# Optimization experiments

Measured on AMD Instinct MI355X. Metric: run time of the kernel, lower is better.

The kernel has to match this reference:

```python
import jax, jax.numpy as jnp
import numpy as np
from jax import lax

RF = 19       # receptive field: layers*(kernel-1)+1 = 3*6+1
WINDOW = 12
N_MIX = 2
K = 20        # subgraph_size (top-k per row)
GDEP = 2
ALPHA = 0.05  # propalpha
EPS = 1e-5


def conv2d(x, w, b):
    # x: [N,C,H,W], w: [O,I,1,k], valid conv along time (last) axis
    o = lax.conv_general_dilated(x, w, (1, 1), 'VALID',
                                 dimension_numbers=('NCHW', 'OIHW', 'NCHW'))
    return o + b[None, :, None, None]


def dilated_inception(x, ws, b):
    # ws: kernels [co, ci, k] for k in (2,3,6,7); dilation factor is 1 here
    outs = [lax.conv_general_dilated(x, w[:, :, None, :], (1, 1), 'VALID',
                                     dimension_numbers=('NCHW', 'OIHW', 'NCHW'))
            for w in ws]
    L = outs[-1].shape[-1]  # truncate to shortest (largest kernel) length
    out = jnp.concatenate([o[..., -L:] for o in outs], axis=1)
    return out + b[None, :, None, None]


def build_adj(e1, e2, l1w, l1b, l2w, l2b):
    # e1,e2: [M2,N,D] embedding tables (idx = arange -> full table)
    # torch Linear: y = x @ W.T + b, W: [out,in]
    nv1 = jnp.einsum('mnd,mod->mno', e1, l1w) + l1b[:, None, :]
    nv2 = jnp.einsum('mnd,mod->mno', e2, l2w) + l2b[:, None, :]
    a = jnp.einsum('mnd,mkd->mnk', nv1, nv2)  # [M2, N, N] per-block adjacency
    rows = [jnp.concatenate([a[i * N_MIX + j] for j in range(N_MIX)], axis=1)
            for i in range(N_MIX)]
    adj = jnp.concatenate(rows, axis=0)  # [NT, NT]
    _, t = lax.top_k(adj, K)  # per-row top-k indices
    mask = jnp.zeros_like(adj).at[jnp.arange(adj.shape[0])[:, None], t].set(1.0)
    return adj * mask


def mixprop(x, adj, w, b):
    a = adj + jnp.eye(adj.shape[0], dtype=adj.dtype)
    a = a / jnp.sum(a, axis=1, keepdims=True)  # row-normalize
    h = x
    outs = [h]
    for _ in range(GDEP):
        h = ALPHA * x + (1.0 - ALPHA) * jnp.einsum('ncwl,vw->ncvl', h, a)
        outs.append(h)
    ho = jnp.concatenate(outs, axis=1)  # [B,(GDEP+1)*C,V,L]
    return jnp.einsum('ncvl,oc->novl', ho, w) + b[None, :, None, None]


def layernorm(x, w, b):
    # torch F.layer_norm over all dims except batch; idx = arange -> full affine
    mu = jnp.mean(x, axis=(1, 2, 3), keepdims=True)
    var = jnp.mean((x - mu) ** 2, axis=(1, 2, 3), keepdims=True)
    return (x - mu) * lax.rsqrt(var + EPS) * w[None] + b[None]


def setup_inputs() -> dict:
    keys = iter(jax.random.split(jax.random.key(0), 80))
    def rn(shape, s=0.1):
        return s * jax.random.normal(next(keys), shape, dtype=jnp.float32)
    d = {}
    d['x_in'] = jax.random.normal(next(keys), (32, 12, 500, 4), dtype=jnp.float32)
    d['start_w'] = rn((32, 1, 1, 1)); d['start_b'] = rn((32,))
    d['skip0_w'] = rn((64, 1, 1, 19)); d['skip0_b'] = rn((64,))
    d['emb1'] = rn((3, 4, 500, 40)); d['emb2'] = rn((3, 4, 500, 40))
    d['lin1_w'] = rn((3, 4, 40, 40)); d['lin1_b'] = rn((3, 4, 40))
    d['lin2_w'] = rn((3, 4, 40, 40)); d['lin2_b'] = rn((3, 4, 40))
    d['g1_w'] = rn((3, 32, 96)); d['g1_b'] = rn((3, 32))
    d['g2_w'] = rn((3, 32, 96)); d['g2_b'] = rn((3, 32))
    for pref in ('filt', 'gate'):
        for k in (2, 3, 6, 7):
            d[f'{pref}_w{k}'] = rn((3, 8, 32, k))
        d[f'{pref}_b'] = rn((3, 32))
    for i, L in zip((1, 2, 3), (13, 7, 1)):
        d[f'skip_w{i}'] = rn((64, 32, 1, L)); d[f'skip_b{i}'] = rn((64,))
        d[f'norm_w{i}'] = jnp.ones((32, 1000, L), jnp.float32)
        d[f'norm_b{i}'] = jnp.zeros((32, 1000, L), jnp.float32)
    d['skipE_w'] = rn((64, 32, 1, 1)); d['skipE_b'] = rn((64,))
    d['end1_w'] = rn((128, 64, 1, 1)); d['end1_b'] = rn((128,))
    d['end2_w'] = rn((12, 128, 1, 1)); d['end2_b'] = rn((12,))
    return d


def reference(x_in, start_w, start_b, skip0_w, skip0_b, emb1, emb2,
              lin1_w, lin1_b, lin2_w, lin2_b, g1_w, g1_b, g2_w, g2_b,
              filt_w2, filt_w3, filt_w6, filt_w7, filt_b,
              gate_w2, gate_w3, gate_w6, gate_w7, gate_b,
              skip_w1, skip_b1, skip_w2, skip_b2, skip_w3, skip_b3,
              norm_w1, norm_b1, norm_w2, norm_b2, norm_w3, norm_b3,
              skipE_w, skipE_b, end1_w, end1_b, end2_w, end2_b):
    feat = x_in[..., :-2]  # drop last 2 'time' features
    # split per-mode feature and stack along node dim: [B,T,2N,1]
    inp = jnp.concatenate([feat[..., 0:1], feat[..., 1:2]], axis=2)
    inp = jnp.transpose(inp, (0, 3, 2, 1))  # [B,1,2N,T]
    inp = jnp.pad(inp, ((0, 0), (0, 0), (0, 0), (RF - WINDOW, 0)))
    x = conv2d(inp, start_w, start_b)       # [B,32,1000,19]
    skip = conv2d(inp, skip0_w, skip0_b)    # [B,64,1000,1] (dropout=eval no-op)
    filt_ws = (filt_w2, filt_w3, filt_w6, filt_w7)
    gate_ws = (gate_w2, gate_w3, gate_w6, gate_w7)
    skips = ((skip_w1, skip_b1), (skip_w2, skip_b2), (skip_w3, skip_b3))
    norms = ((norm_w1, norm_b1), (norm_w2, norm_b2), (norm_w3, norm_b3))
    for i in range(3):
        adp = build_adj(emb1[i], emb2[i], lin1_w[i], lin1_b[i], lin2_w[i], lin2_b[i])
        residual = x
        x = mixprop(x, adp, g1_w[i], g1_b[i]) + mixprop(x, adp.T, g2_w[i], g2_b[i])
        f = jnp.tanh(dilated_inception(x, [w[i] for w in filt_ws], filt_b[i]))
        g = jax.nn.sigmoid(dilated_inception(x, [w[i] for w in gate_ws], gate_b[i]))
        x = f * g
        sw, sb = skips[i]
        skip = conv2d(x, sw, sb) + skip
        x = x + residual[..., -x.shape[3]:]
        nw, nb = norms[i]
        x = layernorm(x, nw, nb)
    skip = conv2d(x, skipE_w, skipE_b) + skip
    x = jax.nn.relu(skip)
    x = jax.nn.relu(conv2d(x, end1_w, end1_b))
    return conv2d(x, end2_w, end2_b)  # [B, horizon*out_dim0=12, 1000, 1]
```

## Files before the change

kernel.cpp:

```cpp
#include <hip/hip_runtime.h>
#include <math.h>


#define ALPHA_C 0.05f
#define EPS_C 1e-5f
#define NBC 32
#define CSCT_CAP 140000

__device__ float g_inp[32 * 19 * 1000];
__device__ float g_skip[32 * 64 * 1000];
__device__ float g_nv1[240000];
__device__ float g_nv2[240000];
__device__ __align__(16) int   g_tkcol[60000];
__device__ __align__(16) float g_tkval[60000];
__device__ float g_inv1[3000];
__device__ int   g_colcnt[3000];
__device__ float g_colsum[3000];
__device__ int   g_rp2[3 * 1001 + 1];
__device__ int   g_fill[3000];
__device__ int   g_cscr[60000];
__device__ float g_cscv[60000];
__device__ float g_inv2[3000];
__device__ float g_stats[3 * 64];
__device__ __align__(16) int2 g_pk1T[60000];
__device__ __align__(16) int2 g_cscT[3 * CSCT_CAP];
__device__ int   g_perm[3 * 1024];
__device__ int   g_degT[3 * 1024];
__device__ int   g_iperm[3 * 1000];
__device__ int   g_tOff[3 * 17];
__device__ float g_B0[(size_t)NBC * 32 * 19 * 1000];
__device__ float g_B1[(size_t)NBC * 32 * 19 * 1000];
__device__ float g_B2[(size_t)NBC * 32 * 19 * 1000];
__device__ float g_B3[(size_t)NBC * 32 * 19 * 1000];
__device__ float g_B4[(size_t)NBC * 32 * 19 * 1000];
__device__ float g_B5[(size_t)NBC * 32 * 19 * 1000];

__device__ __forceinline__ float* bufsel(int s)
{
    switch (s) {
        case 0: return g_B0;
        case 1: return g_B1;
        case 2: return g_B2;
        case 3: return g_B3;
        case 4: return g_B4;
        default: return g_B5;
    }
}

__global__ void k_init()
{
    int i = blockIdx.x * 256 + threadIdx.x;
    if (i < 3000) { g_colcnt[i] = 0; g_colsum[i] = 0.f; g_fill[i] = 0; }
    if (i < 192) g_stats[i] = 0.f;
}

__global__ void k_out_zero(float* __restrict__ out, int n)
{
    int i = blockIdx.x * 256 + threadIdx.x;
    if (i < n) out[i] = 0.0f;
}

__global__ void k_marker(float* __restrict__ out, float v)
{
    if (threadIdx.x == 0) out[0] = v;
}


__global__ void k_build_inp(const float* __restrict__ xin)
{
    int i = blockIdx.x * 256 + threadIdx.x;
    if (i >= 32 * 19 * 1000) return;
    int v = i % 1000;
    int t = (i / 1000) % 19;
    int b = i / 19000;
    float val = 0.f;
    if (t >= 7) {
        int tt = t - 7;
        int n = (v < 500) ? v : v - 500;
        int f = (v < 500) ? 0 : 1;
        val = xin[((b * 12 + tt) * 500 + n) * 4 + f];
    }
    g_inp[i] = val;
}

__global__ void k_nv(const float* __restrict__ e1, const float* __restrict__ e2,
                     const float* __restrict__ w1, const float* __restrict__ b1,
                     const float* __restrict__ w2, const float* __restrict__ b2)
{
    int i = blockIdx.x * 256 + threadIdx.x;
    if (i >= 12 * 500 * 40) return;
    int o = i % 40;
    int n = (i / 40) % 500;
    int m = i / (40 * 500);
    const float* p1 = e1 + (m * 500 + n) * 40;
    const float* pw1 = w1 + (m * 40 + o) * 40;
    const float* p2 = e2 + (m * 500 + n) * 40;
    const float* pw2 = w2 + (m * 40 + o) * 40;
    float a1 = b1[m * 40 + o], a2 = b2[m * 40 + o];
    for (int d = 0; d < 40; ++d) {
        a1 += p1[d] * pw1[d];
        a2 += p2[d] * pw2[d];
    }
    g_nv1[i] = a1;
    g_nv2[i] = a2;
}

__global__ __launch_bounds__(256) void k_adj_topk()
{
    __shared__ float row[1000];
    __shared__ float rv[256];
    __shared__ int ri[256];
    __shared__ int selc[20];
    __shared__ float selv[20];
    int li = blockIdx.x / 1000;
    int r = blockIdx.x % 1000;
    int tid = threadIdx.x;
    int bi = r / 500, n = r % 500;
    for (int c = tid; c < 1000; c += 256) {
        int bj = c / 500, k = c % 500;
        int mg = li * 4 + 2 * bi + bj;
        const float* a = g_nv1 + (mg * 500 + n) * 40;
        const float* b = g_nv2 + (mg * 500 + k) * 40;
        float acc = 0.f;
#pragma unroll
        for (int d = 0; d < 40; ++d) acc += a[d] * b[d];
        row[c] = acc;
    }
    __syncthreads();
    for (int sel = 0; sel < 20; ++sel) {
        float bv = -INFINITY;
        int bidx = 0;
        for (int c = tid; c < 1000; c += 256) {
            float x = row[c];
            if (x > bv) { bv = x; bidx = c; }
        }
        rv[tid] = bv;
        ri[tid] = bidx;
        __syncthreads();
        for (int s = 128; s > 0; s >>= 1) {
            if (tid < s) {
                float ov = rv[tid + s];
                int oi = ri[tid + s];
                if (ov > rv[tid] || (ov == rv[tid] && oi < ri[tid])) { rv[tid] = ov; ri[tid] = oi; }
            }
            __syncthreads();
        }
        if (tid == 0) {
            int ci = ri[0];
            if (ci < 0 || ci > 999) ci = sel;
            selc[sel] = ci;
            selv[sel] = rv[0];
            g_tkcol[(li * 1000 + r) * 20 + sel] = ci;
            g_tkval[(li * 1000 + r) * 20 + sel] = rv[0];
            row[ci] = -INFINITY;
        }
        __syncthreads();
    }
    if (tid < 20) {
        atomicAdd(&g_colcnt[li * 1000 + selc[tid]], 1);
        atomicAdd(&g_colsum[li * 1000 + selc[tid]], selv[tid]);
    }
    if (tid == 0) {
        float s = 0.f;
        for (int j = 0; j < 20; ++j) s += selv[j];
        g_inv1[li * 1000 + r] = 1.f / (s + 1.f);
    }
}

__global__ __launch_bounds__(256) void k_scan()
{
    __shared__ int s[1000];
    int li = blockIdx.x;
    int tid = threadIdx.x;
    for (int i = tid; i < 1000; i += 256) s[i] = g_colcnt[li * 1000 + i];
    __syncthreads();
    if (tid == 0) {
        int run = 0;
        for (int i = 0; i < 1000; ++i) { int c = s[i]; s[i] = run; run += c; }
        g_rp2[li * 1001 + 1000] = run;
    }
    __syncthreads();
    for (int i = tid; i < 1000; i += 256) {
        g_rp2[li * 1001 + i] = s[i];
        g_inv2[li * 1000 + i] = 1.f / (g_colsum[li * 1000 + i] + 1.f);
    }
}

__global__ __launch_bounds__(256) void k_permsort()
{
    __shared__ int deg[1000];
    __shared__ int tmax[16];
    int li = blockIdx.x;
    int tid = threadIdx.x;
    for (int v = tid; v < 1000; v += 256)
        deg[v] = g_rp2[li * 1001 + v + 1] - g_rp2[li * 1001 + v];
    __syncthreads();
    for (int v = tid; v < 1000; v += 256) {
        int d = deg[v];
        int r = 0;
        for (int u = 0; u < 1000; ++u) {
            int du = deg[u];
            r += (du > d) || (du == d && u < v);
        }
        g_perm[li * 1024 + r] = v;
        g_degT[li * 1024 + r] = d;
        g_iperm[li * 1000 + v] = r;
        if ((r & 63) == 0) tmax[r >> 6] = d;
    }
    if (tid < 24) {
        g_perm[li * 1024 + 1000 + tid] = -1;
        g_degT[li * 1024 + 1000 + tid] = 0;
    }
    __syncthreads();
    if (tid == 0) {
        int off = 0;
        for (int t = 0; t < 16; ++t) {
            g_tOff[li * 17 + t] = off;
            off += 64 * tmax[t];
        }
        g_tOff[li * 17 + 16] = off;
    }
}

__global__ void k_scatter()
{
    int i = blockIdx.x * 256 + threadIdx.x;
    if (i >= 3 * 20000) return;
    int li = i / 20000;
    int e = i % 20000;
    int r = e / 20;
    int c = g_tkcol[i];
    if (c < 0) c = 0;
    if (c > 999) c = 999;
    float v = g_tkval[i];
    int pos = g_rp2[li * 1001 + c] + atomicAdd(&g_fill[li * 1000 + c], 1);
    if (pos < 0) pos = 0;
    if (pos > 19999) pos = 19999;
    g_cscr[li * 20000 + pos] = r;
    g_cscv[li * 20000 + pos] = v;
}

__global__ void k_packT1()
{
    int i = blockIdx.x * 256 + threadIdx.x;
    if (i >= 60000) return;
    int li = i / 20000;
    int e = i % 20000;
    int v = e / 20, j = e % 20;
    int c1 = g_tkcol[i];
    if (c1 < 0) c1 = 0;
    if (c1 > 999) c1 = 999;
    g_pk1T[li * 20000 + j * 1000 + v] = make_int2(c1 * 16, __float_as_int(g_tkval[i]));
}

__global__ void k_packT2()
{
    int i = blockIdx.x * 256 + threadIdx.x;
    if (i >= 3000) return;
    int li = i / 1000, v = i % 1000;
    int r = g_iperm[li * 1000 + v];
    int t = r >> 6, ln = r & 63;
    int j0 = g_rp2[li * 1001 + v];
    int d = g_rp2[li * 1001 + v + 1] - j0;
    int base = g_tOff[li * 17 + t];
    for (int j = 0; j < d; ++j) {
        int row = g_cscr[li * 20000 + j0 + j];
        if (row < 0) row = 0;
        if (row > 999) row = 999;
        int pos = base + j * 64 + ln;
        if (pos >= 0 && pos < CSCT_CAP)
            g_cscT[li * CSCT_CAP + pos] =
                make_int2(row * 16, __float_as_int(g_cscv[li * 20000 + j0 + j]));
    }
}


__global__ void k_start(const float* __restrict__ sw, const float* __restrict__ sb, int xsel)
{
    float* X = bufsel(xsel);
    long long i = (long long)blockIdx.x * 256 + threadIdx.x;
    if (i >= (long long)NBC * 32 * 19 * 1000) return;
    int v = (int)(i % 1000);
    int t = (int)((i / 1000) % 19);
    int c = (int)((i / 19000) % 32);
    int bl = (int)(i / (19000LL * 32));
    X[i] = sw[c] * g_inp[(bl * 19 + t) * 1000 + v] + sb[c];
}

__global__ __launch_bounds__(256) void k_skip0(const float* __restrict__ w,
                                               const float* __restrict__ bb)
{
    __shared__ float s_inp[19 * 32];
    __shared__ float s_w[64 * 19];
    int b = blockIdx.y;
    int v0 = blockIdx.x * 32;
    int tid = threadIdx.x;
    for (int i = tid; i < 64 * 19; i += 256) s_w[i] = w[i];
    for (int i = tid; i < 19 * 32; i += 256) {
        int t = i / 32, vl = i % 32;
        int v = v0 + vl;
        s_inp[i] = (v < 1000) ? g_inp[(b * 19 + t) * 1000 + v] : 0.f;
    }
    __syncthreads();
    for (int e = tid; e < 64 * 32; e += 256) {
        int o = e / 32, vl = e % 32;
        int v = v0 + vl;
        if (v >= 1000) continue;
        float acc = bb[o];
#pragma unroll
        for (int t = 0; t < 19; ++t) acc += s_w[o * 19 + t] * s_inp[t * 32 + vl];
        g_skip[(b * 64 + o) * 1000 + v] = acc;
    }
}

__global__ __launch_bounds__(256, 5) void k_prop4(int xsel, int o1s, int o2s, int o3s, int o4s,
                                                  int li, int CH)
{
    __shared__ float4 S[2000];
    const float* X = bufsel(xsel);
    float* o1 = bufsel(o1s);
    float* o2 = bufsel(o2s);
    float* o3 = bufsel(o3s);
    float* o4 = bufsel(o4s);
    const int2* pkT = g_pk1T + li * 20000;
    const int2* cT = g_cscT + (size_t)li * CSCT_CAP;
    const int* prm = g_perm + li * 1024;
    const int* dgT = g_degT + li * 1024;
    const int* tOf = g_tOff + li * 17;
    const float* iv1 = g_inv1 + li * 1000;
    const float* iv2 = g_inv2 + li * 1000;
    int n = blockIdx.y;
    int ch0 = blockIdx.x * 4;
    size_t gb = ((size_t)n * CH + ch0) * 1000;
    int tid = threadIdx.x;
    int wv = tid >> 6, lane = tid & 63;
    char* Ub = (char*)S;
    char* Wb = (char*)(S + 1000);
    float4* U4 = S;
    float4* W4 = S + 1000;

    auto csr_hop = [&](const char* sb, float4* dst) {
        for (int it = 0; it < 4; ++it) {
            int v = it * 256 + tid;
            if (v >= 1000) break;
            const int2* mp = pkT + v;
            float4 a = *(const float4*)(sb + (size_t)v * 16);
#pragma unroll
            for (int jb = 0; jb < 5; ++jb) {
                int2 e0 = mp[(jb * 4 + 0) * 1000];
                int2 e1 = mp[(jb * 4 + 1) * 1000];
                int2 e2 = mp[(jb * 4 + 2) * 1000];
                int2 e3 = mp[(jb * 4 + 3) * 1000];
                float w0 = __int_as_float(e0.y), w1 = __int_as_float(e1.y);
                float w2 = __int_as_float(e2.y), w3 = __int_as_float(e3.y);
                float4 x0 = *(const float4*)(sb + e0.x);
                float4 x1 = *(const float4*)(sb + e1.x);
                float4 x2 = *(const float4*)(sb + e2.x);
                float4 x3 = *(const float4*)(sb + e3.x);
                a.x += w0 * x0.x + w1 * x1.x + w2 * x2.x + w3 * x3.x;
                a.y += w0 * x0.y + w1 * x1.y + w2 * x2.y + w3 * x3.y;
                a.z += w0 * x0.z + w1 * x1.z + w2 * x2.z + w3 * x3.z;
                a.w += w0 * x0.w + w1 * x1.w + w2 * x2.w + w3 * x3.w;
            }
            float s = iv1[v];
            a.x *= s; a.y *= s; a.z *= s; a.w *= s;
            dst[v] = a;
        }
    };

    auto csc_hop = [&](const char* sb, float4* dst) {
        for (int o = 0; o < 4; ++o) {
            int tile = o * 4 + ((o & 1) ? (3 - wv) : wv);
            int r = tile * 64 + lane;
            int v = prm[r];
            if (v < 0) continue;
            int d = dgT[r];
            const int2* mp = cT + tOf[tile] + lane;
            float4 a = *(const float4*)(sb + (size_t)v * 16);
            int j = 0;
            for (; j + 4 <= d; j += 4) {
                int2 e0 = mp[(j + 0) * 64];
                int2 e1 = mp[(j + 1) * 64];
                int2 e2 = mp[(j + 2) * 64];
                int2 e3 = mp[(j + 3) * 64];
                float w0 = __int_as_float(e0.y), w1 = __int_as_float(e1.y);
                float w2 = __int_as_float(e2.y), w3 = __int_as_float(e3.y);
                float4 x0 = *(const float4*)(sb + e0.x);
                float4 x1 = *(const float4*)(sb + e1.x);
                float4 x2 = *(const float4*)(sb + e2.x);
                float4 x3 = *(const float4*)(sb + e3.x);
                a.x += w0 * x0.x + w1 * x1.x + w2 * x2.x + w3 * x3.x;
                a.y += w0 * x0.y + w1 * x1.y + w2 * x2.y + w3 * x3.y;
                a.z += w0 * x0.z + w1 * x1.z + w2 * x2.z + w3 * x3.z;
                a.w += w0 * x0.w + w1 * x1.w + w2 * x2.w + w3 * x3.w;
            }
            for (; j < d; ++j) {
                int2 e = mp[j * 64];
                float w = __int_as_float(e.y);
                float4 x = *(const float4*)(sb + e.x);
                a.x += w * x.x; a.y += w * x.y; a.z += w * x.z; a.w += w * x.w;
            }
            float s = iv2[v];
            a.x *= s; a.y *= s; a.z *= s; a.w *= s;
            dst[v] = a;
        }
    };

    for (int it = 0; it < 4; ++it) {
        int v = it * 256 + tid;
        if (v >= 1000) break;
        float4 t;
        t.x = X[gb + v];
        t.y = X[gb + 1000 + v];
        t.z = X[gb + 2000 + v];
        t.w = X[gb + 3000 + v];
        U4[v] = t;
    }
    __syncthreads();

    csr_hop(Ub, W4);
    __syncthreads();

    for (int it = 0; it < 4; ++it) {
        int v = it * 256 + tid;
        if (v >= 1000) break;
        float4 t = W4[v];
        o1[gb + v] = t.x;
        o1[gb + 1000 + v] = t.y;
        o1[gb + 2000 + v] = t.z;
        o1[gb + 3000 + v] = t.w;
    }
    csr_hop(Wb, U4);
    __syncthreads();

    for (int it = 0; it < 4; ++it) {
        int v = it * 256 + tid;
        if (v >= 1000) break;
        float4 t = U4[v];
        o2[gb + v] = t.x;
        o2[gb + 1000 + v] = t.y;
        o2[gb + 2000 + v] = t.z;
        o2[gb + 3000 + v] = t.w;
        float4 x;
        x.x = X[gb + v];
        x.y = X[gb + 1000 + v];
        x.z = X[gb + 2000 + v];
        x.w = X[gb + 3000 + v];
        W4[v] = x;
    }
    __syncthreads();

    csc_hop(Wb, U4);
    __syncthreads();

    for (int it = 0; it < 4; ++it) {
        int v = it * 256 + tid;
        if (v >= 1000) break;
        float4 t = U4[v];
        o3[gb + v] = t.x;
        o3[gb + 1000 + v] = t.y;
        o3[gb + 2000 + v] = t.z;
        o3[gb + 3000 + v] = t.w;
    }
    csc_hop(Ub, W4);
    __syncthreads();

    for (int it = 0; it < 4; ++it) {
        int v = it * 256 + tid;
        if (v >= 1000) break;
        float4 t = W4[v];
        o4[gb + v] = t.x;
        o4[gb + 1000 + v] = t.y;
        o4[gb + 2000 + v] = t.z;
        o4[gb + 3000 + v] = t.w;
    }
}

__global__ __launch_bounds__(256) void k_mix(int xs, int h1s, int h2s, int h3s, int h4s, int ms,
                                             const float* __restrict__ g1w, const float* __restrict__ g2w,
                                             const float* __restrict__ g1b, const float* __restrict__ g2b,
                                             int P)
{
    __shared__ float sW[5 * 1024];
    __shared__ float sB[32];
    int tid = threadIdx.x;
    const float A = ALPHA_C, Bq = 1.f - ALPHA_C;
    for (int i = tid; i < 1024; i += 256) {
        int o = i >> 5, c = i & 31;
        float w1 = g1w[o * 96 + 32 + c], w2 = g1w[o * 96 + 64 + c];
        float w3 = g2w[o * 96 + 32 + c], w4 = g2w[o * 96 + 64 + c];
        sW[i]        = g1w[o * 96 + c] + g2w[o * 96 + c] + A * (w1 + w2 + w3 + w4);
        sW[1024 + i] = Bq * (w1 + A * w2);
        sW[2048 + i] = Bq * Bq * w2;
        sW[3072 + i] = Bq * (w3 + A * w4);
        sW[4096 + i] = Bq * Bq * w4;
    }
    if (tid < 32) sB[tid] = g1b[tid] + g2b[tid];
    __syncthreads();
    int n = blockIdx.y;
    int p = blockIdx.x * 256 + tid;
    if (p >= P) return;
    const float* srcs[5] = {bufsel(xs), bufsel(h1s), bufsel(h2s), bufsel(h3s), bufsel(h4s)};
    float acc[32];
#pragma unroll
    for (int o = 0; o < 32; ++o) acc[o] = sB[o];
    for (int st = 0; st < 5; ++st) {
        const float* src = srcs[st] + (size_t)n * 32 * P + p;
        const float* w = &sW[st * 1024];
        for (int c = 0; c < 32; ++c) {
            float hv = src[(size_t)c * P];
#pragma unroll
            for (int o = 0; o < 32; ++o) acc[o] += w[o * 32 + c] * hv;
        }
    }
    float* XM = bufsel(ms) + (size_t)n * 32 * P + p;
#pragma unroll
    for (int o = 0; o < 32; ++o) XM[(size_t)o * P] = acc[o];
}

template <int LIN>
__global__ __launch_bounds__(256) void k_incept(int xmsel, int xgsel,
                                                const float* __restrict__ fw2, const float* __restrict__ fw3,
                                                const float* __restrict__ fw6, const float* __restrict__ fw7,
                                                const float* __restrict__ fb,
                                                const float* __restrict__ gw2, const float* __restrict__ gw3,
                                                const float* __restrict__ gw6, const float* __restrict__ gw7,
                                                const float* __restrict__ gb,
                                                const float* __restrict__ skw, const float* __restrict__ skb)
{
    const int LOUT = LIN - 6;
    const float* XM = bufsel(xmsel);
    float* XG = bufsel(xgsel);
    __shared__ float sx[32 * 8 * LIN];
    __shared__ float sxg[32 * 8 * LOUT];
    int tid = threadIdx.x;
    int n = blockIdx.y, v0 = blockIdx.x * 8;
    for (int i = tid; i < 32 * LIN * 8; i += 256) {
        int vl = i & 7;
        int l = (i >> 3) % LIN;
        int c = i / (8 * LIN);
        sx[(c * 8 + vl) * LIN + l] = XM[(((size_t)n * 32 + c) * LIN + l) * 1000 + v0 + vl];
    }
    __syncthreads();
    int co = tid >> 3, vl = tid & 7;
    int s = co >> 3, co_s = co & 7;
    const int ksz[4] = {2, 3, 6, 7};
    int k = ksz[s];
    const float* fw = (s == 0) ? fw2 : ((s == 1) ? fw3 : ((s == 2) ? fw6 : fw7));
    const float* gw = (s == 0) ? gw2 : ((s == 1) ? gw3 : ((s == 2) ? gw6 : gw7));
    float accf[LOUT], accg[LOUT];
    float bf = fb[co], bg = gb[co];
#pragma unroll
    for (int l = 0; l < LOUT; ++l) { accf[l] = bf; accg[l] = bg; }
    for (int c = 0; c < 32; ++c) {
        const float* xp = &sx[(c * 8 + vl) * LIN];
        for (int j = 0; j < k; ++j) {
            float wf = fw[(co_s * 32 + c) * k + j];
            float wg = gw[(co_s * 32 + c) * k + j];
            int base = 7 - k + j;
#pragma unroll
            for (int l = 0; l < LOUT; ++l) {
                float xv = xp[base + l];
                accf[l] += wf * xv;
                accg[l] += wg * xv;
            }
        }
    }
    size_t ob = ((size_t)n * 32 + co) * LOUT * 1000 + v0 + vl;
#pragma unroll
    for (int l = 0; l < LOUT; ++l) {
        float g = tanhf(accf[l]) * (1.f / (1.f + expf(-accg[l])));
        XG[ob + (size_t)l * 1000] = g;
        sxg[(co * 8 + vl) * LOUT + l] = g;
    }
    __syncthreads();
    int obk = tid >> 3;
    for (int half = 0; half < 2; ++half) {
        int o = obk + 32 * half;
        float acc = skb[o];
        for (int c = 0; c < 32; ++c) {
            const float* wp = &skw[((size_t)o * 32 + c) * LOUT];
            const float* xp = &sxg[(c * 8 + vl) * LOUT];
#pragma unroll
            for (int l = 0; l < LOUT; ++l) acc += wp[l] * xp[l];
        }
        size_t si = ((size_t)n * 64 + o) * 1000 + v0 + vl;
        g_skip[si] += acc;
    }
}

__global__ __launch_bounds__(256) void k_resid_stats(int xnsel, int xpsel,
                                                     int li, int LIN, int LOUT)
{
    float* XN = bufsel(xnsel);
    const float* Xp = bufsel(xpsel);
    float* stats = g_stats + li * 64;
    int n = blockIdx.y;
    int S = 32 * LOUT * 1000;
    int tid = threadIdx.x;
    int gsz = gridDim.x * 256;
    float sum = 0.f, ss = 0.f;
    for (int idx = blockIdx.x * 256 + tid; idx < S; idx += gsz) {
        int v = idx % 1000;
        int l = (idx / 1000) % LOUT;
        int c = idx / (1000 * LOUT);
        float y = XN[(size_t)n * S + idx] +
                  Xp[(((size_t)n * 32 + c) * LIN + l + (LIN - LOUT)) * 1000 + v];
        XN[(size_t)n * S + idx] = y;
        sum += y;
        ss += y * y;
    }
    __shared__ float s1[256], s2[256];
    s1[tid] = sum;
    s2[tid] = ss;
    __syncthreads();
    for (int s = 128; s > 0; s >>= 1) {
        if (tid < s) { s1[tid] += s1[tid + s]; s2[tid] += s2[tid + s]; }
        __syncthreads();
    }
    if (tid == 0) {
        atomicAdd(&stats[n * 2], s1[0]);
        atomicAdd(&stats[n * 2 + 1], s2[0]);
    }
}

__global__ void k_norm(int xnsel, const float* __restrict__ nw,
                       const float* __restrict__ nb, int li, int LOUT)
{
    float* XN = bufsel(xnsel);
    const float* stats = g_stats + li * 64;
    int S = 32 * LOUT * 1000;
    long long i = (long long)blockIdx.x * 256 + threadIdx.x;
    if (i >= (long long)NBC * S) return;
    int n = (int)(i / S);
    int rem = (int)(i % S);
    int v = rem % 1000;
    int l = (rem / 1000) % LOUT;
    int c = rem / (1000 * LOUT);
    int widx = (c * 1000 + v) * LOUT + l;
    float cnt = (float)S;
    float mu = stats[n * 2] / cnt;
    float var = stats[n * 2 + 1] / cnt - mu * mu;
    float rs = rsqrtf(var + EPS_C);
    XN[i] = (XN[i] - mu) * rs * nw[widx] + nb[widx];
}

__global__ __launch_bounds__(256) void k_final(int xsel,
                                               const float* __restrict__ ew, const float* __restrict__ eb,
                                               const float* __restrict__ e1w, const float* __restrict__ e1b,
                                               const float* __restrict__ e2w, const float* __restrict__ e2b,
                                               float* __restrict__ out)
{
    const float* X = bufsel(xsel);
    __shared__ float sxf[32 * 16];
    __shared__ float sk[64 * 16];
    __shared__ float s1[64 * 16];
    __shared__ float s2[128 * 16];
    int b = blockIdx.y, v0 = blockIdx.x * 16;
    int tid = threadIdx.x;
    for (int i = tid; i < 512; i += 256) {
        int c = i / 16, vl = i & 15;
        int v = v0 + vl;
        sxf[i] = (v < 1000) ? X[((size_t)b * 32 + c) * 1000 + v] : 0.f;
    }
    for (int i = tid; i < 1024; i += 256) {
        int o = i / 16, vl = i & 15;
        int v = v0 + vl;
        sk[i] = (v < 1000) ? g_skip[((size_t)b * 64 + o) * 1000 + v] : 0.f;
    }
    __syncthreads();
    for (int i = tid; i < 1024; i += 256) {
        int o = i / 16, vl = i & 15;
        float acc = sk[i] + eb[o];
        for (int c = 0; c < 32; ++c) acc += ew[o * 32 + c] * sxf[c * 16 + vl];
        s1[i] = fmaxf(acc, 0.f);
    }
    __syncthreads();
    for (int i = tid; i < 2048; i += 256) {
        int o = i / 16, vl = i & 15;
        float acc = e1b[o];
        for (int c = 0; c < 64; ++c) acc += e1w[o * 64 + c] * s1[c * 16 + vl];
        s2[i] = fmaxf(acc, 0.f);
    }
    __syncthreads();
    if (tid < 192) {
        int o = tid / 16, vl = tid & 15;
        int v = v0 + vl;
        if (v < 1000) {
            float acc = e2b[o];
            for (int c = 0; c < 128; ++c) acc += e2w[o * 128 + c] * s2[c * 16 + vl];
            out[((size_t)b * 12 + o) * 1000 + v] = acc;
        }
    }
}


static const int SZ_SORT[43] = {240000,240000,128,8192,12,1536,96,1536,2304,4608,
                                5376,96,9216,96,9216,96,1536,2304,4608,5376,
                                480,19200,480,19200,416000,224000,32000,416000,224000,32000,
                                64,1216,64,2048,64,64,64,26624,14336,2048,32,32,768000};
static const int SZ_DICT[43] = {768000,32,32,1216,64,240000,240000,19200,480,19200,
                                480,9216,96,9216,96,1536,2304,4608,5376,96,
                                1536,2304,4608,5376,96,26624,64,416000,416000,14336,
                                64,224000,224000,2048,64,32000,32000,2048,64,8192,128,1536,12};
static const int SZ_SIG[43]  = {768000,32,32,1216,64,240000,240000,19200,480,19200,
                                480,9216,96,9216,96,1536,2304,4608,5376,96,
                                1536,2304,4608,5376,96,26624,64,14336,64,2048,
                                64,416000,416000,224000,224000,32000,32000,2048,64,8192,128,1536,12};

extern "C" void kernel_launch(void* const* d_in, const int* in_sizes, int n_in,
                              void* d_out, int out_size, void* d_ws, size_t ws_size,
                              hipStream_t stream)
{
    (void)d_ws; (void)ws_size;
    const float *x_in, *start_w, *start_b, *skip0_w, *skip0_b;
    const float *emb1, *emb2, *lin1_w, *lin1_b, *lin2_w, *lin2_b;
    const float *g1_w, *g1_b, *g2_w, *g2_b;
    const float *filt_w[4], *filt_b, *gate_w[4], *gate_b;
    const float *skw[3], *skb[3], *nww[3], *nbb[3];
    const float *skipE_w, *skipE_b, *end1_w, *end1_b, *end2_w, *end2_b;
    float* outp = (float*)d_out;
    auto P = [&](int i) { return (const float*)d_in[i]; };
    auto match = [&](const int* tab) {
        if (n_in < 43) return false;
        for (int i = 0; i < 43; ++i) if (in_sizes[i] != tab[i]) return false;
        return true;
    };

    int fam = -1;
    if (match(SZ_SORT)) fam = 0;
    else if (match(SZ_DICT)) fam = 1;
    else if (match(SZ_SIG)) fam = 2;

    if (fam == 0) {
        emb1 = P(0); emb2 = P(1); end1_b = P(2); end1_w = P(3); end2_b = P(4); end2_w = P(5);
        filt_b = P(6); filt_w[0] = P(7); filt_w[1] = P(8); filt_w[2] = P(9); filt_w[3] = P(10);
        g1_b = P(11); g1_w = P(12); g2_b = P(13); g2_w = P(14);
        gate_b = P(15); gate_w[0] = P(16); gate_w[1] = P(17); gate_w[2] = P(18); gate_w[3] = P(19);
        lin1_b = P(20); lin1_w = P(21); lin2_b = P(22); lin2_w = P(23);
        nbb[0] = P(24); nbb[1] = P(25); nbb[2] = P(26);
        nww[0] = P(27); nww[1] = P(28); nww[2] = P(29);
        skip0_b = P(30); skip0_w = P(31); skipE_b = P(32); skipE_w = P(33);
        skb[0] = P(34); skb[1] = P(35); skb[2] = P(36);
        skw[0] = P(37); skw[1] = P(38); skw[2] = P(39);
        start_b = P(40); start_w = P(41); x_in = P(42);
    } else if (fam == 1 || fam == 2) {
        x_in = P(0); start_w = P(1); start_b = P(2); skip0_w = P(3); skip0_b = P(4);
        emb1 = P(5); emb2 = P(6); lin1_w = P(7); lin1_b = P(8); lin2_w = P(9); lin2_b = P(10);
        g1_w = P(11); g1_b = P(12); g2_w = P(13); g2_b = P(14);
        filt_w[0] = P(15); filt_w[1] = P(16); filt_w[2] = P(17); filt_w[3] = P(18); filt_b = P(19);
        gate_w[0] = P(20); gate_w[1] = P(21); gate_w[2] = P(22); gate_w[3] = P(23); gate_b = P(24);
        if (fam == 1) {
            skw[0] = P(25); skb[0] = P(26); nww[0] = P(27); nbb[0] = P(28);
            skw[1] = P(29); skb[1] = P(30); nww[1] = P(31); nbb[1] = P(32);
            skw[2] = P(33); skb[2] = P(34); nww[2] = P(35); nbb[2] = P(36);
        } else {
            skw[0] = P(25); skb[0] = P(26); skw[1] = P(27); skb[1] = P(28);
            skw[2] = P(29); skb[2] = P(30);
            nww[0] = P(31); nbb[0] = P(32); nww[1] = P(33); nbb[1] = P(34);
            nww[2] = P(35); nbb[2] = P(36);
        }
        skipE_w = P(37); skipE_b = P(38); end1_w = P(39); end1_b = P(40);
        end2_w = P(41); end2_b = P(42);
    } else {
        k_out_zero<<<(out_size + 255) / 256, 256, 0, stream>>>(outp, out_size);
        k_marker<<<1, 64, 0, stream>>>(outp, 8192.0f);
        return;
    }

    k_init<<<12, 256, 0, stream>>>();
    k_build_inp<<<(32 * 19 * 1000 + 255) / 256, 256, 0, stream>>>(x_in);
    k_nv<<<(240000 + 255) / 256, 256, 0, stream>>>(emb1, emb2, lin1_w, lin1_b, lin2_w, lin2_b);
    k_adj_topk<<<3000, 256, 0, stream>>>();
    k_scan<<<3, 256, 0, stream>>>();
    k_permsort<<<3, 256, 0, stream>>>();
    k_scatter<<<(60000 + 255) / 256, 256, 0, stream>>>();
    k_packT1<<<(60000 + 255) / 256, 256, 0, stream>>>();
    k_packT2<<<12, 256, 0, stream>>>();

    int X = 0;
    long long big = (long long)NBC * 32 * 19 * 1000;
    k_start<<<(unsigned)((big + 255) / 256), 256, 0, stream>>>(start_w, start_b, X);
    k_skip0<<<dim3(32, NBC), 256, 0, stream>>>(skip0_w, skip0_b);

    int LIN = 19;
    for (int li = 0; li < 3; ++li) {
        int LOUT = LIN - 6;
        int Pp = 1000 * LIN;
        int hb[4], hn = 0;
        for (int b = 0; b < 6 && hn < 4; ++b)
            if (b != X && b != 1) hb[hn++] = b;
        int h1 = hb[0], h2 = hb[1], h3 = hb[2], h4 = hb[3];
        int CH = 32 * LIN;
        dim3 gg((unsigned)(CH / 4), NBC);

        k_prop4<<<gg, 256, 0, stream>>>(X, h1, h2, h3, h4, li, CH);

        k_mix<<<dim3((Pp + 255) / 256, NBC), 256, 0, stream>>>(X, h1, h2, h3, h4, 1,
            g1_w + li * 3072, g2_w + li * 3072, g1_b + li * 32, g2_b + li * 32, Pp);

        int XG = h1;
        if (LIN == 19)
            k_incept<19><<<dim3(125, NBC), 256, 0, stream>>>(1, XG,
                filt_w[0] + li * 512, filt_w[1] + li * 768, filt_w[2] + li * 1536, filt_w[3] + li * 1792,
                filt_b + li * 32,
                gate_w[0] + li * 512, gate_w[1] + li * 768, gate_w[2] + li * 1536, gate_w[3] + li * 1792,
                gate_b + li * 32, skw[li], skb[li]);
        else if (LIN == 13)
            k_incept<13><<<dim3(125, NBC), 256, 0, stream>>>(1, XG,
                filt_w[0] + li * 512, filt_w[1] + li * 768, filt_w[2] + li * 1536, filt_w[3] + li * 1792,
                filt_b + li * 32,
                gate_w[0] + li * 512, gate_w[1] + li * 768, gate_w[2] + li * 1536, gate_w[3] + li * 1792,
                gate_b + li * 32, skw[li], skb[li]);
        else
            k_incept<7><<<dim3(125, NBC), 256, 0, stream>>>(1, XG,
                filt_w[0] + li * 512, filt_w[1] + li * 768, filt_w[2] + li * 1536, filt_w[3] + li * 1792,
                filt_b + li * 32,
                gate_w[0] + li * 512, gate_w[1] + li * 768, gate_w[2] + li * 1536, gate_w[3] + li * 1792,
                gate_b + li * 32, skw[li], skb[li]);

        k_resid_stats<<<dim3(16, NBC), 256, 0, stream>>>(XG, X, li, LIN, LOUT);
        long long tot = (long long)NBC * 32 * LOUT * 1000;
        k_norm<<<(unsigned)((tot + 255) / 256), 256, 0, stream>>>(XG, nww[li], nbb[li], li, LOUT);

        X = XG;
        LIN = LOUT;
    }
    k_final<<<dim3(63, NBC), 256, 0, stream>>>(X, skipE_w, skipE_b,
                                               end1_w, end1_b, end2_w, end2_b, outp);
}
```

Baseline: 2.777 ms.

## Fuse start conv into layer-0 consumers, wave-shuffle top-k, dual-row CSR hop

```diff
diff --git a/kernel.cpp b/kernel.cpp
--- a/kernel.cpp
+++ b/kernel.cpp
@@ -108,13 +108,14 @@
 __global__ __launch_bounds__(256) void k_adj_topk()
 {
     __shared__ float row[1000];
-    __shared__ float rv[256];
-    __shared__ int ri[256];
+    __shared__ float wvv[4];
+    __shared__ int wvi[4];
     __shared__ int selc[20];
     __shared__ float selv[20];
     int li = blockIdx.x / 1000;
     int r = blockIdx.x % 1000;
     int tid = threadIdx.x;
+    int wv = tid >> 6, lane = tid & 63;
     int bi = r / 500, n = r % 500;
     for (int c = tid; c < 1000; c += 256) {
         int bj = c / 500, k = c % 500;
@@ -134,24 +135,29 @@
             float x = row[c];
             if (x > bv) { bv = x; bidx = c; }
         }
-        rv[tid] = bv;
-        ri[tid] = bidx;
+#pragma unroll
+        for (int m = 1; m < 64; m <<= 1) {
+            float ov = __shfl_xor(bv, m);
+            int oi = __shfl_xor(bidx, m);
+            if (ov > bv || (ov == bv && oi < bidx)) { bv = ov; bidx = oi; }
+        }
+        if (lane == 0) { wvv[wv] = bv; wvi[wv] = bidx; }
         __syncthreads();
-        for (int s = 128; s > 0; s >>= 1) {
-            if (tid < s) {
-                float ov = rv[tid + s];
-                int oi = ri[tid + s];
-                if (ov > rv[tid] || (ov == rv[tid] && oi < ri[tid])) { rv[tid] = ov; ri[tid] = oi; }
+        if (tid == 0) {
+            float fv = wvv[0];
+            int fi = wvi[0];
+#pragma unroll
+            for (int k = 1; k < 4; ++k) {
+                float ov = wvv[k];
+                int oi = wvi[k];
+                if (ov > fv || (ov == fv && oi < fi)) { fv = ov; fi = oi; }
             }
-            __syncthreads();
-        }
-        if (tid == 0) {
-            int ci = ri[0];
+            int ci = fi;
             if (ci < 0 || ci > 999) ci = sel;
             selc[sel] = ci;
-            selv[sel] = rv[0];
+            selv[sel] = fv;
             g_tkcol[(li * 1000 + r) * 20 + sel] = ci;
-            g_tkval[(li * 1000 + r) * 20 + sel] = rv[0];
+            g_tkval[(li * 1000 + r) * 20 + sel] = fv;
             row[ci] = -INFINITY;
         }
         __syncthreads();
@@ -275,18 +281,6 @@
 }
 
 
-__global__ void k_start(const float* __restrict__ sw, const float* __restrict__ sb, int xsel)
-{
-    float* X = bufsel(xsel);
-    long long i = (long long)blockIdx.x * 256 + threadIdx.x;
-    if (i >= (long long)NBC * 32 * 19 * 1000) return;
-    int v = (int)(i % 1000);
-    int t = (int)((i / 1000) % 19);
-    int c = (int)((i / 19000) % 32);
-    int bl = (int)(i / (19000LL * 32));
-    X[i] = sw[c] * g_inp[(bl * 19 + t) * 1000 + v] + sb[c];
-}
-
 __global__ __launch_bounds__(256) void k_skip0(const float* __restrict__ w,
                                                const float* __restrict__ bb)
 {
@@ -314,7 +308,9 @@
 }
 
 __global__ __launch_bounds__(256, 5) void k_prop4(int xsel, int o1s, int o2s, int o3s, int o4s,
-                                                  int li, int CH)
+                                                  int li, int CH, int li0,
+                                                  const float* __restrict__ sw,
+                                                  const float* __restrict__ sb)
 {
     __shared__ float4 S[2000];
     const float* X = bufsel(xsel);
@@ -338,37 +334,59 @@
     char* Wb = (char*)(S + 1000);
     float4* U4 = S;
     float4* W4 = S + 1000;
-
-    auto csr_hop = [&](const char* sb, float4* dst) {
-        for (int it = 0; it < 4; ++it) {
-            int v = it * 256 + tid;
-            if (v >= 1000) break;
-            const int2* mp = pkT + v;
-            float4 a = *(const float4*)(sb + (size_t)v * 16);
+    float4 xr[4];
+
+    auto csr_hop = [&](const char* sbuf, float4* dst) {
+#pragma unroll
+        for (int half = 0; half < 2; ++half) {
+            int u0 = half * 512 + tid;
+            int u1 = u0 + 256;
+            int v0 = (u0 > 999) ? 999 : u0;
+            int v1 = (u1 > 999) ? 999 : u1;
+            const int2* mp0 = pkT + v0;
+            const int2* mp1 = pkT + v1;
+            float4 a0 = *(const float4*)(sbuf + (size_t)v0 * 16);
+            float4 a1 = *(const float4*)(sbuf + (size_t)v1 * 16);
 #pragma unroll
             for (int jb = 0; jb < 5; ++jb) {
-                int2 e0 = mp[(jb * 4 + 0) * 1000];
-                int2 e1 = mp[(jb * 4 + 1) * 1000];
-                int2 e2 = mp[(jb * 4 + 2) * 1000];
-                int2 e3 = mp[(jb * 4 + 3) * 1000];
+                int2 e0 = mp0[(jb * 4 + 0) * 1000];
+                int2 e1 = mp0[(jb * 4 + 1) * 1000];
+                int2 e2 = mp0[(jb * 4 + 2) * 1000];
+                int2 e3 = mp0[(jb * 4 + 3) * 1000];
+                int2 f0 = mp1[(jb * 4 + 0) * 1000];
+                int2 f1 = mp1[(jb * 4 + 1) * 1000];
+                int2 f2 = mp1[(jb * 4 + 2) * 1000];
+                int2 f3 = mp1[(jb * 4 + 3) * 1000];
+                float4 x0 = *(const float4*)(sbuf + e0.x);
+                float4 x1 = *(const float4*)(sbuf + e1.x);
+                float4 x2 = *(const float4*)(sbuf + e2.x);
+                float4 x3 = *(const float4*)(sbuf + e3.x);
+                float4 y0 = *(const float4*)(sbuf + f0.x);
+                float4 y1 = *(const float4*)(sbuf + f1.x);
+                float4 y2 = *(const float4*)(sbuf + f2.x);
+                float4 y3 = *(const float4*)(sbuf + f3.x);
                 float w0 = __int_as_float(e0.y), w1 = __int_as_float(e1.y);
                 float w2 = __int_as_float(e2.y), w3 = __int_as_float(e3.y);
-                float4 x0 = *(const float4*)(sb + e0.x);
-                float4 x1 = *(const float4*)(sb + e1.x);
-                float4 x2 = *(const float4*)(sb + e2.x);
-                float4 x3 = *(const float4*)(sb + e3.x);
-                a.x += w0 * x0.x + w1 * x1.x + w2 * x2.x + w3 * x3.x;
-                a.y += w0 * x0.y + w1 * x1.y + w2 * x2.y + w3 * x3.y;
-                a.z += w0 * x0.z + w1 * x1.z + w2 * x2.z + w3 * x3.z;
-                a.w += w0 * x0.w + w1 * x1.w + w2 * x2.w + w3 * x3.w;
+                float q0 = __int_as_float(f0.y), q1 = __int_as_float(f1.y);
+                float q2 = __int_as_float(f2.y), q3 = __int_as_float(f3.y);
+                a0.x += w0 * x0.x + w1 * x1.x + w2 * x2.x + w3 * x3.x;
+                a0.y += w0 * x0.y + w1 * x1.y + w2 * x2.y + w3 * x3.y;
+                a0.z += w0 * x0.z + w1 * x1.z + w2 * x2.z + w3 * x3.z;
+                a0.w += w0 * x0.w + w1 * x1.w + w2 * x2.w + w3 * x3.w;
+                a1.x += q0 * y0.x + q1 * y1.x + q2 * y2.x + q3 * y3.x;
+                a1.y += q0 * y0.y + q1 * y1.y + q2 * y2.y + q3 * y3.y;
+                a1.z += q0 * y0.z + q1 * y1.z + q2 * y2.z + q3 * y3.z;
+                a1.w += q0 * y0.w + q1 * y1.w + q2 * y2.w + q3 * y3.w;
             }
-            float s = iv1[v];
-            a.x *= s; a.y *= s; a.z *= s; a.w *= s;
-            dst[v] = a;
+            float s0 = iv1[v0], s1 = iv1[v1];
+            a0.x *= s0; a0.y *= s0; a0.z *= s0; a0.w *= s0;
+            a1.x *= s1; a1.y *= s1; a1.z *= s1; a1.w *= s1;
+            dst[v0] = a0;
+            dst[v1] = a1;
         }
     };
 
-    auto csc_hop = [&](const char* sb, float4* dst) {
+    auto csc_hop = [&](const char* sbuf, float4* dst) {
         for (int o = 0; o < 4; ++o) {
             int tile = o * 4 + ((o & 1) ? (3 - wv) : wv);
             int r = tile * 64 + lane;
@@ -376,7 +394,7 @@
             if (v < 0) continue;
             int d = dgT[r];
             const int2* mp = cT + tOf[tile] + lane;
-            float4 a = *(const float4*)(sb + (size_t)v * 16);
+            float4 a = *(const float4*)(sbuf + (size_t)v * 16);
             int j = 0;
             for (; j + 4 <= d; j += 4) {
                 int2 e0 = mp[(j + 0) * 64];
@@ -385,10 +403,10 @@
                 int2 e3 = mp[(j + 3) * 64];
                 float w0 = __int_as_float(e0.y), w1 = __int_as_float(e1.y);
                 float w2 = __int_as_float(e2.y), w3 = __int_as_float(e3.y);
-                float4 x0 = *(const float4*)(sb + e0.x);
-                float4 x1 = *(const float4*)(sb + e1.x);
-                float4 x2 = *(const float4*)(sb + e2.x);
-                float4 x3 = *(const float4*)(sb + e3.x);
+                float4 x0 = *(const float4*)(sbuf + e0.x);
+                float4 x1 = *(const float4*)(sbuf + e1.x);
+                float4 x2 = *(const float4*)(sbuf + e2.x);
+                float4 x3 = *(const float4*)(sbuf + e3.x);
                 a.x += w0 * x0.x + w1 * x1.x + w2 * x2.x + w3 * x3.x;
                 a.y += w0 * x0.y + w1 * x1.y + w2 * x2.y + w3 * x3.y;
                 a.z += w0 * x0.z + w1 * x1.z + w2 * x2.z + w3 * x3.z;
@@ -397,7 +415,7 @@
             for (; j < d; ++j) {
                 int2 e = mp[j * 64];
                 float w = __int_as_float(e.y);
-                float4 x = *(const float4*)(sb + e.x);
+                float4 x = *(const float4*)(sbuf + e.x);
                 a.x += w * x.x; a.y += w * x.y; a.z += w * x.z; a.w += w * x.w;
             }
             float s = iv2[v];
@@ -406,83 +424,117 @@
         }
     };
 
+    if (li0) {
+        float swv0 = sw[(ch0 + 0) / 19], sbv0 = sb[(ch0 + 0) / 19];
+        float swv1 = sw[(ch0 + 1) / 19], sbv1 = sb[(ch0 + 1) / 19];
+        float swv2 = sw[(ch0 + 2) / 19], sbv2 = sb[(ch0 + 2) / 19];
+        float swv3 = sw[(ch0 + 3) / 19], sbv3 = sb[(ch0 + 3) / 19];
+        const float* i0 = g_inp + (n * 19 + (ch0 + 0) % 19) * 1000;
+        const float* i1 = g_inp + (n * 19 + (ch0 + 1) % 19) * 1000;
+        const float* i2 = g_inp + (n * 19 + (ch0 + 2) % 19) * 1000;
+        const float* i3 = g_inp + (n * 19 + (ch0 + 3) % 19) * 1000;
+#pragma unroll
+        for (int it = 0; it < 4; ++it) {
+            int v = it * 256 + tid;
+            if (v < 1000) {
+                float4 t;
+                t.x = swv0 * i0[v] + sbv0;
+                t.y = swv1 * i1[v] + sbv1;
+                t.z = swv2 * i2[v] + sbv2;
+                t.w = swv3 * i3[v] + sbv3;
+                U4[v] = t;
+                xr[it] = t;
+            }
+        }
+    } else {
+#pragma unroll
+        for (int it = 0; it < 4; ++it) {
+            int v = it * 256 + tid;
+            if (v < 1000) {
+                float4 t;
+                t.x = X[gb + v];
+                t.y = X[gb + 1000 + v];
+                t.z = X[gb + 2000 + v];
+                t.w = X[gb + 3000 + v];
+                U4[v] = t;
+                xr[it] = t;
+            }
+        }
+    }
+    __syncthreads();
+
+    csr_hop(Ub, W4);
+    __syncthreads();
+
+#pragma unroll
     for (int it = 0; it < 4; ++it) {
         int v = it * 256 + tid;
-        if (v >= 1000) break;
-        float4 t;
-        t.x = X[gb + v];
-        t.y = X[gb + 1000 + v];
-        t.z = X[gb + 2000 + v];
-        t.w = X[gb + 3000 + v];
-        U4[v] = t;
-    }
-    __syncthreads();
-
-    csr_hop(Ub, W4);
-    __syncthreads();
-
+        if (v < 1000) {
+            float4 t = W4[v];
+            o1[gb + v] = t.x;
+            o1[gb + 1000 + v] = t.y;
+            o1[gb + 2000 + v] = t.z;
+            o1[gb + 3000 + v] = t.w;
+        }
+    }
+    csr_hop(Wb, U4);
+    __syncthreads();
+
+#pragma unroll
     for (int it = 0; it < 4; ++it) {
         int v = it * 256 + tid;
-        if (v >= 1000) break;
-        float4 t = W4[v];
-        o1[gb + v] = t.x;
-        o1[gb + 1000 + v] = t.y;
-        o1[gb + 2000 + v] = t.z;
-        o1[gb + 3000 + v] = t.w;
-    }
-    csr_hop(Wb, U4);
-    __syncthreads();
-
+        if (v < 1000) {
+            float4 t = U4[v];
+            o2[gb + v] = t.x;
+            o2[gb + 1000 + v] = t.y;
+            o2[gb + 2000 + v] = t.z;
+            o2[gb + 3000 + v] = t.w;
+            W4[v] = xr[it];
+        }
+    }
+    __syncthreads();
+
+    csc_hop(Wb, U4);
+    __syncthreads();
+
+#pragma unroll
     for (int it = 0; it < 4; ++it) {
         int v = it * 256 + tid;
-        if (v >= 1000) break;
-        float4 t = U4[v];
-        o2[gb + v] = t.x;
-        o2[gb + 1000 + v] = t.y;
-        o2[gb + 2000 + v] = t.z;
-        o2[gb + 3000 + v] = t.w;
-        float4 x;
-        x.x = X[gb + v];
-        x.y = X[gb + 1000 + v];
-        x.z = X[gb + 2000 + v];
-        x.w = X[gb + 3000 + v];
-        W4[v] = x;
-    }
-    __syncthreads();
-
-    csc_hop(Wb, U4);
-    __syncthreads();
-
+        if (v < 1000) {
+            float4 t = U4[v];
+            o3[gb + v] = t.x;
+            o3[gb + 1000 + v] = t.y;
+            o3[gb + 2000 + v] = t.z;
+            o3[gb + 3000 + v] = t.w;
+        }
+    }
+    csc_hop(Ub, W4);
+    __syncthreads();
+
+#pragma unroll
     for (int it = 0; it < 4; ++it) {
         int v = it * 256 + tid;
-        if (v >= 1000) break;
-        float4 t = U4[v];
-        o3[gb + v] = t.x;
-        o3[gb + 1000 + v] = t.y;
-        o3[gb + 2000 + v] = t.z;
-        o3[gb + 3000 + v] = t.w;
-    }
-    csc_hop(Ub, W4);
-    __syncthreads();
-
-    for (int it = 0; it < 4; ++it) {
-        int v = it * 256 + tid;
-        if (v >= 1000) break;
-        float4 t = W4[v];
-        o4[gb + v] = t.x;
-        o4[gb + 1000 + v] = t.y;
-        o4[gb + 2000 + v] = t.z;
-        o4[gb + 3000 + v] = t.w;
+        if (v < 1000) {
+            float4 t = W4[v];
+            o4[gb + v] = t.x;
+            o4[gb + 1000 + v] = t.y;
+            o4[gb + 2000 + v] = t.z;
+            o4[gb + 3000 + v] = t.w;
+        }
     }
 }
 
 __global__ __launch_bounds__(256) void k_mix(int xs, int h1s, int h2s, int h3s, int h4s, int ms,
                                              const float* __restrict__ g1w, const float* __restrict__ g2w,
                                              const float* __restrict__ g1b, const float* __restrict__ g2b,
-                                             int P)
+                                             int P, int li0,
+                                             const float* __restrict__ sw_,
+                                             const float* __restrict__ sb_)
 {
     __shared__ float sW[5 * 1024];
     __shared__ float sB[32];
+    __shared__ float sWS[32];
+    __shared__ float sSB[32];
     int tid = threadIdx.x;
     const float A = ALPHA_C, Bq = 1.f - ALPHA_C;
     for (int i = tid; i < 1024; i += 256) {
@@ -497,14 +549,34 @@
     }
     if (tid < 32) sB[tid] = g1b[tid] + g2b[tid];
     __syncthreads();
+    if (li0 && tid < 32) {
+        float as = 0.f, ab = 0.f;
+        for (int c = 0; c < 32; ++c) {
+            float w = sW[tid * 32 + c];
+            as += w * sw_[c];
+            ab += w * sb_[c];
+        }
+        sWS[tid] = as;
+        sSB[tid] = ab;
+    }
+    if (li0) __syncthreads();
     int n = blockIdx.y;
     int p = blockIdx.x * 256 + tid;
     if (p >= P) return;
     const float* srcs[5] = {bufsel(xs), bufsel(h1s), bufsel(h2s), bufsel(h3s), bufsel(h4s)};
     float acc[32];
-#pragma unroll
-    for (int o = 0; o < 32; ++o) acc[o] = sB[o];
-    for (int st = 0; st < 5; ++st) {
+    int st0;
+    if (li0) {
+        float xv = g_inp[(size_t)n * 19000 + p];
+#pragma unroll
+        for (int o = 0; o < 32; ++o) acc[o] = sB[o] + sSB[o] + sWS[o] * xv;
+        st0 = 1;
+    } else {
+#pragma unroll
+        for (int o = 0; o < 32; ++o) acc[o] = sB[o];
+        st0 = 0;
+    }
+    for (int st = st0; st < 5; ++st) {
         const float* src = srcs[st] + (size_t)n * 32 * P + p;
         const float* w = &sW[st * 1024];
         for (int c = 0; c < 32; ++c) {
@@ -590,7 +662,9 @@
 }
 
 __global__ __launch_bounds__(256) void k_resid_stats(int xnsel, int xpsel,
-                                                     int li, int LIN, int LOUT)
+                                                     int li, int LIN, int LOUT, int li0,
+                                                     const float* __restrict__ sw_,
+                                                     const float* __restrict__ sb_)
 {
     float* XN = bufsel(xnsel);
     const float* Xp = bufsel(xpsel);
@@ -604,8 +678,12 @@
         int v = idx % 1000;
         int l = (idx / 1000) % LOUT;
         int c = idx / (1000 * LOUT);
-        float y = XN[(size_t)n * S + idx] +
-                  Xp[(((size_t)n * 32 + c) * LIN + l + (LIN - LOUT)) * 1000 + v];
+        float r;
+        if (li0)
+            r = sw_[c] * g_inp[(n * 19 + l + 6) * 1000 + v] + sb_[c];
+        else
+            r = Xp[(((size_t)n * 32 + c) * LIN + l + (LIN - LOUT)) * 1000 + v];
+        float y = XN[(size_t)n * S + idx] + r;
         XN[(size_t)n * S + idx] = y;
         sum += y;
         ss += y * y;
@@ -778,15 +856,14 @@
     k_packT1<<<(60000 + 255) / 256, 256, 0, stream>>>();
     k_packT2<<<12, 256, 0, stream>>>();
 
+    k_skip0<<<dim3(32, NBC), 256, 0, stream>>>(skip0_w, skip0_b);
+
     int X = 0;
-    long long big = (long long)NBC * 32 * 19 * 1000;
-    k_start<<<(unsigned)((big + 255) / 256), 256, 0, stream>>>(start_w, start_b, X);
-    k_skip0<<<dim3(32, NBC), 256, 0, stream>>>(skip0_w, skip0_b);
-
     int LIN = 19;
     for (int li = 0; li < 3; ++li) {
         int LOUT = LIN - 6;
         int Pp = 1000 * LIN;
+        int li0 = (li == 0) ? 1 : 0;
         int hb[4], hn = 0;
         for (int b = 0; b < 6 && hn < 4; ++b)
             if (b != X && b != 1) hb[hn++] = b;
@@ -794,10 +871,11 @@
         int CH = 32 * LIN;
         dim3 gg((unsigned)(CH / 4), NBC);
 
-        k_prop4<<<gg, 256, 0, stream>>>(X, h1, h2, h3, h4, li, CH);
+        k_prop4<<<gg, 256, 0, stream>>>(X, h1, h2, h3, h4, li, CH, li0, start_w, start_b);
 
         k_mix<<<dim3((Pp + 255) / 256, NBC), 256, 0, stream>>>(X, h1, h2, h3, h4, 1,
-            g1_w + li * 3072, g2_w + li * 3072, g1_b + li * 32, g2_b + li * 32, Pp);
+            g1_w + li * 3072, g2_w + li * 3072, g1_b + li * 32, g2_b + li * 32, Pp,
+            li0, start_w, start_b);
 
         int XG = h1;
         if (LIN == 19)
@@ -819,7 +897,8 @@
                 gate_w[0] + li * 512, gate_w[1] + li * 768, gate_w[2] + li * 1536, gate_w[3] + li * 1792,
                 gate_b + li * 32, skw[li], skb[li]);
 
-        k_resid_stats<<<dim3(16, NBC), 256, 0, stream>>>(XG, X, li, LIN, LOUT);
+        k_resid_stats<<<dim3(16, NBC), 256, 0, stream>>>(XG, X, li, LIN, LOUT,
+                                                         li0, start_w, start_b);
         long long tot = (long long)NBC * 32 * LOUT * 1000;
         k_norm<<<(unsigned)((tot + 255) / 256), 256, 0, stream>>>(XG, nww[li], nbb[li], li, LOUT);
 
```

New measurement: 3.035 ms. +9.3%, slower.
